# Kernel tuning notes

Measured on AMD Instinct MI355X. Metric: run time of the kernel, lower is better.

The kernel has to match this reference:

```python
import jax, jax.numpy as jnp
import numpy as np

D_MODEL = 1024
N_HEADS = 16
D_HEAD = D_MODEL // N_HEADS
D_FF = 2048
B, S = 4, 1024
EPS = 1e-6


def layernorm(x, gamma, beta):
    mu = jnp.mean(x, axis=-1, keepdims=True)
    var = jnp.mean(jnp.square(x - mu), axis=-1, keepdims=True)
    return (x - mu) * jax.lax.rsqrt(var + EPS) * gamma + beta


def setup_inputs() -> dict:
    key = jax.random.key(0)
    ks = jax.random.split(key, 12)
    s = 0.02
    return {
        "x": jax.random.normal(ks[0], (B, S, D_MODEL), jnp.float32),
        "mask": jnp.ones((B, 1, 1, S), jnp.int32),
        "Wq": jax.random.normal(ks[1], (D_MODEL, D_MODEL), jnp.float32) * s,
        "Wk": jax.random.normal(ks[2], (D_MODEL, D_MODEL), jnp.float32) * s,
        "Wv": jax.random.normal(ks[3], (D_MODEL, D_MODEL), jnp.float32) * s,
        "Wo": jax.random.normal(ks[4], (D_MODEL, D_MODEL), jnp.float32) * s,
        "bo": jnp.zeros((D_MODEL,), jnp.float32),
        "ln1_g": jnp.ones((D_MODEL,), jnp.float32),
        "ln1_b": jnp.zeros((D_MODEL,), jnp.float32),
        "W1": jax.random.normal(ks[5], (D_MODEL, D_FF), jnp.float32) * s,
        "b1": jnp.zeros((D_FF,), jnp.float32),
        "W2": jax.random.normal(ks[6], (D_FF, D_MODEL), jnp.float32) * s,
        "b2": jnp.zeros((D_MODEL,), jnp.float32),
        "ln2_g": jnp.ones((D_MODEL,), jnp.float32),
        "ln2_b": jnp.zeros((D_MODEL,), jnp.float32),
    }


def reference(x, mask, Wq, Wk, Wv, Wo, bo, ln1_g, ln1_b, W1, b1, W2, b2, ln2_g, ln2_b):
    b, s, _ = x.shape
    # --- multi-head attention ---
    q_proj = x @ Wq                      # [B,S,D]
    k_proj = x @ Wk
    v_proj = x @ Wv
    q = q_proj.reshape(b, s, N_HEADS, D_HEAD)
    k = k_proj.reshape(b, s, N_HEADS, D_HEAD)
    v = v_proj.reshape(b, s, N_HEADS, D_HEAD)
    attn = jnp.einsum('bqhd,bkhd->bhqk', q, k)           # [B,H,S,S]
    attn = jnp.where(mask == 0, -jnp.inf, attn)
    attn = jax.nn.softmax(attn / jnp.sqrt(jnp.float32(D_MODEL)), axis=-1)
    out = jnp.einsum('bhqk,bkhd->bqhd', attn, v).reshape(b, s, D_MODEL)
    # source applies ReLU after the output projection, dropout=eval identity
    out = jax.nn.relu(out @ Wo + bo) + q_proj            # residual = projected queries
    out = layernorm(out, ln1_g, ln1_b)
    # --- FFN (source applies activation AFTER linear2) ---
    ff = jax.nn.relu((out @ W1 + b1) @ W2 + b2) + out
    return layernorm(ff, ln2_g, ln2_b)
```

## Files before the change

kernel.cpp:

```cpp
#include <hip/hip_runtime.h>
#include <hip/hip_bf16.h>

#define D_MODEL 1024
#define N_HEADS 16
#define D_HEAD  64
#define D_FF    2048
#define BATCH   4
#define SEQ     1024
#define ROWS    (BATCH*SEQ)

typedef __bf16  bf16x8 __attribute__((ext_vector_type(8)));
typedef float   f32x4  __attribute__((ext_vector_type(4)));
typedef unsigned int u32x4 __attribute__((ext_vector_type(4)));
typedef unsigned int u32x2 __attribute__((ext_vector_type(2)));
typedef unsigned short u16;
typedef unsigned int u32;

__device__ inline u16 f2bf(float x){ __hip_bfloat16 b = __float2bfloat16(x); return *(u16*)&b; }

__device__ inline void load_lds16(const u16* gsrc, u16* ldst){
  __builtin_amdgcn_global_load_lds((const __attribute__((address_space(1))) void*)gsrc,
                                   (__attribute__((address_space(3))) void*)ldst, 16, 0, 0);
}

__global__ __launch_bounds__(256)
void cast_bf16_kernel(const float* __restrict__ src, __hip_bfloat16* __restrict__ dst, int n){
  int i = (blockIdx.x*blockDim.x + threadIdx.x)*4;
  if (i + 3 < n){
    float4 v = *(const float4*)(src + i);
    dst[i+0] = __float2bfloat16(v.x);
    dst[i+1] = __float2bfloat16(v.y);
    dst[i+2] = __float2bfloat16(v.z);
    dst[i+3] = __float2bfloat16(v.w);
  }
}

__global__ __launch_bounds__(256)
void transpose_cast_kernel(const float* __restrict__ src, __hip_bfloat16* __restrict__ dst,
                           int R, int C){
  __shared__ float tile[32][33];
  int c0 = blockIdx.x*32, r0 = blockIdx.y*32;
  int tx = threadIdx.x & 31, ty = threadIdx.x >> 5;
  #pragma unroll
  for (int i=0;i<32;i+=8)
    tile[ty+i][tx] = src[(size_t)(r0+ty+i)*C + (c0+tx)];
  __syncthreads();
  #pragma unroll
  for (int i=0;i<32;i+=8)
    dst[(size_t)(c0+ty+i)*R + (r0+tx)] = __float2bfloat16(tile[tx][ty+i]);
}

__global__ __launch_bounds__(256)
void transpose4_kernel(const float* __restrict__ s0, const float* __restrict__ s1,
                       const float* __restrict__ s2, const float* __restrict__ s3,
                       __hip_bfloat16* __restrict__ dst){
  __shared__ float tile[32][33];
  const float* src = (blockIdx.z==0)?s0:(blockIdx.z==1)?s1:(blockIdx.z==2)?s2:s3;
  __hip_bfloat16* d = dst + (size_t)blockIdx.z*1024*1024;
  int c0 = blockIdx.x*32, r0 = blockIdx.y*32;
  int tx = threadIdx.x & 31, ty = threadIdx.x >> 5;
  #pragma unroll
  for (int i=0;i<32;i+=8)
    tile[ty+i][tx] = src[(size_t)(r0+ty+i)*1024 + (c0+tx)];
  __syncthreads();
  #pragma unroll
  for (int i=0;i<32;i+=8)
    d[(size_t)(c0+ty+i)*1024 + (r0+tx)] = __float2bfloat16(tile[tx][ty+i]);
}

template<int MODE>
__global__ __launch_bounds__(256, 2)
void gemm_bt_kernel(const u16* __restrict__ A, const u16* __restrict__ BT,
                    const float* __restrict__ bias, float* __restrict__ Cf,
                    __hip_bfloat16* __restrict__ Cb, int M, int N, int K, float cscale){
  __shared__ u16 As[2][128*32];
  __shared__ u16 Bs[2][128*32];
  const int m0 = blockIdx.y*128, n0 = blockIdx.x*128;
  const int t = threadIdx.x;
  const int wid = t>>6, lane = t&63;
  const int wm = wid>>1, wn = wid&1;
  const int lr = lane&15, lk = (lane>>4)*8;
  const int srow = t>>2, sseg = (t&3)*8;
  const int wbase = wid*512;

  f32x4 acc[4][4] = {};

  for (int kt=0; kt<K; kt+=64){
    __syncthreads();
    #pragma unroll
    for (int half=0; half<2; ++half){
      #pragma unroll
      for (int c=0;c<2;++c){
        load_lds16(A  + (size_t)(m0 + c*64 + srow)*K + kt + half*32 + sseg, &As[half][c*2048 + wbase]);
        load_lds16(BT + (size_t)(n0 + c*64 + srow)*K + kt + half*32 + sseg, &Bs[half][c*2048 + wbase]);
      }
    }
    __syncthreads();
    #pragma unroll
    for (int half=0; half<2; ++half){
      bf16x8 af[4], bfr[4];
      #pragma unroll
      for (int f=0; f<4; ++f){
        af[f]  = *(const bf16x8*)&As[half][(wm*64 + f*16 + lr)*32 + lk];
        bfr[f] = *(const bf16x8*)&Bs[half][(wn*64 + f*16 + lr)*32 + lk];
      }
      #pragma unroll
      for (int i=0;i<4;++i)
        #pragma unroll
        for (int j=0;j<4;++j)
          acc[i][j] = __builtin_amdgcn_mfma_f32_16x16x32_bf16(af[i], bfr[j], acc[i][j], 0,0,0);
    }
  }

  const int r_in = (lane>>4)*4;
  #pragma unroll
  for (int i=0;i<4;++i){
    #pragma unroll
    for (int j=0;j<4;++j){
      int col = n0 + wn*64 + j*16 + lr;
      float bv = bias ? bias[col] : 0.f;
      #pragma unroll
      for (int e=0;e<4;++e){
        int row = m0 + wm*64 + i*16 + r_in + e;
        float v = acc[i][j][e] + bv;
        if (MODE == 0){
          Cf[(size_t)row*N + col] = v;
        } else if (MODE == 1){
          Cb[(size_t)row*N + col] = __float2bfloat16(v);
        } else {
          int b = row>>10, s = row&1023;
          int which = col>>10, c = col&1023, h = c>>6, d = c&63;
          size_t hm = (((size_t)b*16 + h)*1024 + s)*64 + d;
          if (which == 0){
            Cf[(size_t)row*1024 + c] = v;
            Cb[hm] = __float2bfloat16(v * cscale);
          } else if (which == 1){
            Cb[4194304u + hm] = __float2bfloat16(v);
          } else {
            Cb[8388608u + (((size_t)b*16 + h)*64 + d)*1024 + s] = __float2bfloat16(v);
          }
        }
      }
    }
  }
}

__global__ __launch_bounds__(512)
void attn_mfma_kernel(const u16* __restrict__ qb, const u16* __restrict__ kb,
                      const u16* __restrict__ vt, const int* __restrict__ mask,
                      __hip_bfloat16* __restrict__ out){
  __shared__ u16 Ks[64*72];
  __shared__ u16 Vs[64*72];
  __shared__ u16 Pl[8][16*72];
  const int t = threadIdx.x;
  const int wid = t>>6, lane = t&63;
  const int lr = lane&15, lg = lane>>4, lk = lg*8;
  const int bh = blockIdx.y;
  const int b = bh>>4, h = bh&15;
  const int q0 = blockIdx.x*128 + wid*16;
  const u16* qbase = qb + (size_t)bh*1024*64;
  const u16* kbase = kb + (size_t)bh*1024*64;
  const u16* vbase = vt + (size_t)bh*64*1024;
  const int* mrow = mask + b*SEQ;

  bf16x8 aq[2];
  aq[0] = *(const bf16x8*)(qbase + (size_t)(q0+lr)*64 + lk);
  aq[1] = *(const bf16x8*)(qbase + (size_t)(q0+lr)*64 + 32 + lk);

  f32x4 osum[4] = {};
  float m1 = -1e30f, l1 = 0.f;

  for (int kt=0; kt<SEQ/64; ++kt){
    const int k0 = kt*64;
    __syncthreads();
    {
      int r = t>>3, sg = (t&7)*8;
      *(u32x4*)&Ks[r*72+sg] = *(const u32x4*)(kbase + (size_t)(k0+r)*64 + sg);
      *(u32x4*)&Vs[r*72+sg] = *(const u32x4*)(vbase + (size_t)r*1024 + k0 + sg);
    }
    __syncthreads();

    unsigned long long bm = __ballot(mrow[k0 + lane] != 0);

    f32x4 sacc[4] = {};
    __builtin_amdgcn_s_setprio(1);
    #pragma unroll
    for (int k4=0;k4<4;++k4){
      #pragma unroll
      for (int dg=0;dg<2;++dg){
        bf16x8 kf = *(const bf16x8*)&Ks[(k4*16+lr)*72 + dg*32 + lk];
        sacc[k4] = __builtin_amdgcn_mfma_f32_16x16x32_bf16(kf, aq[dg], sacc[k4],0,0,0);
      }
    }
    __builtin_amdgcn_s_setprio(0);
    if (bm != ~0ull){
      #pragma unroll
      for (int k4=0;k4<4;++k4)
        #pragma unroll
        for (int e=0;e<4;++e)
          if (!((bm >> (k4*16 + lg*4 + e)) & 1)) sacc[k4][e] = -1e30f;
    }

    float tm = -1e30f;
    #pragma unroll
    for (int k4=0;k4<4;++k4)
      #pragma unroll
      for (int e=0;e<4;++e) tm = fmaxf(tm, sacc[k4][e]);
    tm = fmaxf(tm, __shfl_xor(tm,16));
    tm = fmaxf(tm, __shfl_xor(tm,32));

    float mn = m1, c = 1.f;
    bool need = !__all(tm <= m1 + 8.f);
    if (need){
      mn = fmaxf(m1, tm);
      c  = exp2f(m1 - mn);
      m1 = mn;
    }
    float ps = 0.f;
    #pragma unroll
    for (int k4=0;k4<4;++k4)
      #pragma unroll
      for (int e=0;e<4;++e){ float p = exp2f(sacc[k4][e]-mn); sacc[k4][e]=p; ps+=p; }
    ps += __shfl_xor(ps,16);
    ps += __shfl_xor(ps,32);
    l1 = l1*c + ps;

    if (need){
      float ce[4];
      #pragma unroll
      for (int e=0;e<4;++e) ce[e] = __shfl(c, lg*4+e);
      #pragma unroll
      for (int dt=0;dt<4;++dt)
        #pragma unroll
        for (int e=0;e<4;++e) osum[dt][e] *= ce[e];
    }

    #pragma unroll
    for (int k4=0;k4<4;++k4){
      u32 lo = (u32)f2bf(sacc[k4][0]) | ((u32)f2bf(sacc[k4][1])<<16);
      u32 hi = (u32)f2bf(sacc[k4][2]) | ((u32)f2bf(sacc[k4][3])<<16);
      u32x2 pk; pk[0]=lo; pk[1]=hi;
      *(u32x2*)&Pl[wid][lr*72 + k4*16 + lg*4] = pk;
    }
    __builtin_amdgcn_s_setprio(1);
    #pragma unroll
    for (int dt=0;dt<4;++dt){
      #pragma unroll
      for (int kg=0;kg<2;++kg){
        bf16x8 pa = *(const bf16x8*)&Pl[wid][lr*72 + kg*32 + lk];
        bf16x8 vf = *(const bf16x8*)&Vs[(dt*16+lr)*72 + kg*32 + lk];
        osum[dt] = __builtin_amdgcn_mfma_f32_16x16x32_bf16(pa, vf, osum[dt],0,0,0);
      }
    }
    __builtin_amdgcn_s_setprio(0);
  }
  float li[4];
  #pragma unroll
  for (int e=0;e<4;++e) li[e] = 1.f / __shfl(l1, lg*4+e);
  #pragma unroll
  for (int dt=0;dt<4;++dt){
    int d = dt*16 + lr;
    #pragma unroll
    for (int e=0;e<4;++e){
      int q = q0 + lg*4 + e;
      out[((size_t)b*1024 + q)*1024 + h*64 + d] = __float2bfloat16(osum[dt][e] * li[e]);
    }
  }
}

__global__ __launch_bounds__(256)
void ln_fused_kernel(const float* __restrict__ a, const float* __restrict__ res,
                     const float* __restrict__ g, const float* __restrict__ be,
                     float* __restrict__ outf, __hip_bfloat16* __restrict__ outb){
  int row = blockIdx.x, t = threadIdx.x;
  size_t rb = (size_t)row*D_MODEL;
  float4 av = *(const float4*)(a  + rb + t*4);
  float4 rv = *(const float4*)(res+ rb + t*4);
  float v0 = fmaxf(av.x,0.f)+rv.x;
  float v1 = fmaxf(av.y,0.f)+rv.y;
  float v2 = fmaxf(av.z,0.f)+rv.z;
  float v3 = fmaxf(av.w,0.f)+rv.w;
  float sum = v0+v1+v2+v3;
  float ss  = v0*v0+v1*v1+v2*v2+v3*v3;
  #pragma unroll
  for (int off=32; off; off>>=1){ sum += __shfl_xor(sum,off); ss += __shfl_xor(ss,off); }
  __shared__ float red[8];
  int wid = t>>6, lane = t&63;
  if (lane==0){ red[wid]=sum; red[4+wid]=ss; }
  __syncthreads();
  sum = red[0]+red[1]+red[2]+red[3];
  ss  = red[4]+red[5]+red[6]+red[7];
  float mu  = sum*(1.f/1024.f);
  float var = ss*(1.f/1024.f) - mu*mu;
  float rstd = rsqrtf(var + 1e-6f);
  float4 gv = *(const float4*)(g  + t*4);
  float4 bv = *(const float4*)(be + t*4);
  float y0=(v0-mu)*rstd*gv.x+bv.x;
  float y1=(v1-mu)*rstd*gv.y+bv.y;
  float y2=(v2-mu)*rstd*gv.z+bv.z;
  float y3=(v3-mu)*rstd*gv.w+bv.w;
  *(float4*)(outf+rb+t*4) = make_float4(y0,y1,y2,y3);
  if (outb){
    outb[rb+t*4+0]=__float2bfloat16(y0);
    outb[rb+t*4+1]=__float2bfloat16(y1);
    outb[rb+t*4+2]=__float2bfloat16(y2);
    outb[rb+t*4+3]=__float2bfloat16(y3);
  }
}

extern "C" void kernel_launch(void* const* d_in, const int* in_sizes, int n_in,
                              void* d_out, int out_size, void* d_ws, size_t ws_size,
                              hipStream_t stream){
  const float* x    = (const float*)d_in[0];
  const int*   mask = (const int*)  d_in[1];
  const float* Wq   = (const float*)d_in[2];
  const float* Wk   = (const float*)d_in[3];
  const float* Wv   = (const float*)d_in[4];
  const float* Wo   = (const float*)d_in[5];
  const float* bo   = (const float*)d_in[6];
  const float* ln1g = (const float*)d_in[7];
  const float* ln1b = (const float*)d_in[8];
  const float* W1   = (const float*)d_in[9];
  const float* b1   = (const float*)d_in[10];
  const float* W2   = (const float*)d_in[11];
  const float* b2   = (const float*)d_in[12];
  const float* ln2g = (const float*)d_in[13];
  const float* ln2b = (const float*)d_in[14];

  char* ws = (char*)d_ws;
  const size_t MB = 1024*1024;
  __hip_bfloat16* WqT  = (__hip_bfloat16*)(ws + 0);
  __hip_bfloat16* WoT  = (__hip_bfloat16*)(ws + 6*MB);
  __hip_bfloat16* W1T  = (__hip_bfloat16*)(ws + 8*MB);
  __hip_bfloat16* W2T  = (__hip_bfloat16*)(ws + 12*MB);
  __hip_bfloat16* xb   = (__hip_bfloat16*)(ws + 16*MB);
  float* q_proj        = (float*)(ws + 24*MB);
  __hip_bfloat16* qb   = (__hip_bfloat16*)(ws + 40*MB);
  __hip_bfloat16* attn_o = (__hip_bfloat16*)(ws + 64*MB);
  float* proj_o        = (float*)(ws + 40*MB);
  float* h1f           = (float*)(ws + 56*MB);
  __hip_bfloat16* h1b  = (__hip_bfloat16*)(ws + 16*MB);
  __hip_bfloat16* ff1b = (__hip_bfloat16*)(ws + 24*MB);
  float* ff2           = (float*)(ws + 40*MB);

  const float qscale = 0.03125f * 1.44269504f;

  cast_bf16_kernel<<<ROWS*D_MODEL/4/256, 256, 0, stream>>>(x, xb, ROWS*D_MODEL);
  transpose4_kernel<<<dim3(32,32,4), 256, 0, stream>>>(Wq, Wk, Wv, Wo, WqT);
  transpose_cast_kernel<<<dim3(64,32), 256, 0, stream>>>(W1, W1T, 1024, 2048);
  transpose_cast_kernel<<<dim3(32,64), 256, 0, stream>>>(W2, W2T, 2048, 1024);

  gemm_bt_kernel<5><<<dim3(24,32), 256, 0, stream>>>((const u16*)xb, (const u16*)WqT, nullptr,
                                                     q_proj, qb, ROWS, 3072, 1024, qscale);

  attn_mfma_kernel<<<dim3(SEQ/128, BATCH*N_HEADS), 512, 0, stream>>>(
      (const u16*)qb, (const u16*)(qb + 4194304u), (const u16*)(qb + 8388608u), mask, attn_o);

  gemm_bt_kernel<0><<<dim3(8,32), 256, 0, stream>>>((const u16*)attn_o, (const u16*)WoT, bo,
                                                    proj_o, nullptr, ROWS, 1024, 1024, 1.f);

  ln_fused_kernel<<<ROWS, 256, 0, stream>>>(proj_o, q_proj, ln1g, ln1b, h1f, h1b);

  gemm_bt_kernel<1><<<dim3(16,32), 256, 0, stream>>>((const u16*)h1b, (const u16*)W1T, b1,
                                                     nullptr, ff1b, ROWS, 2048, 1024, 1.f);

  gemm_bt_kernel<0><<<dim3(8,32), 256, 0, stream>>>((const u16*)ff1b, (const u16*)W2T, b2,
                                                    ff2, nullptr, ROWS, 1024, 2048, 1.f);

  ln_fused_kernel<<<ROWS, 256, 0, stream>>>(ff2, h1f, ln2g, ln2b, (float*)d_out, nullptr);
}
```

Baseline: 215.7 us.

## Double-buffer attention K/V tiles, remap blocks per XCD, fuse ReLU+residual into GEMM

The attention kernel now double-buffers its K/V tiles in LDS. Each iteration prefetches the next tile into registers and writes it to the alternate buffer after the MFMA work, so only one barrier is needed per iteration. The attention grid is flattened and remapped so that the blocks of one (batch, head) land on the same XCD, which is meant to improve L2 reuse of K/V. The ReLU-plus-residual step moves from the layernorm kernel into a new GEMM epilogue mode, so layernorm no longer reads the residual tensor. In exchange, the attention kernel uses more LDS and registers, and the GEMM epilogue does an extra residual load.

```diff
diff --git a/kernel.cpp b/kernel.cpp
--- a/kernel.cpp
+++ b/kernel.cpp
@@ -71,8 +71,9 @@
 template<int MODE>
 __global__ __launch_bounds__(256, 2)
 void gemm_bt_kernel(const u16* __restrict__ A, const u16* __restrict__ BT,
-                    const float* __restrict__ bias, float* __restrict__ Cf,
-                    __hip_bfloat16* __restrict__ Cb, int M, int N, int K, float cscale){
+                    const float* __restrict__ bias, const float* __restrict__ res,
+                    float* __restrict__ Cf, __hip_bfloat16* __restrict__ Cb,
+                    int M, int N, int K, float cscale){
   __shared__ u16 As[2][128*32];
   __shared__ u16 Bs[2][128*32];
   const int m0 = blockIdx.y*128, n0 = blockIdx.x*128;
@@ -127,6 +128,8 @@
           Cf[(size_t)row*N + col] = v;
         } else if (MODE == 1){
           Cb[(size_t)row*N + col] = __float2bfloat16(v);
+        } else if (MODE == 6){
+          Cf[(size_t)row*N + col] = fmaxf(v,0.f) + res[(size_t)row*N + col];
         } else {
           int b = row>>10, s = row&1023;
           int which = col>>10, c = col&1023, h = c>>6, d = c&63;
@@ -149,15 +152,18 @@
 void attn_mfma_kernel(const u16* __restrict__ qb, const u16* __restrict__ kb,
                       const u16* __restrict__ vt, const int* __restrict__ mask,
                       __hip_bfloat16* __restrict__ out){
-  __shared__ u16 Ks[64*72];
-  __shared__ u16 Vs[64*72];
+  __shared__ u16 Ks[2][64*72];
+  __shared__ u16 Vs[2][64*72];
   __shared__ u16 Pl[8][16*72];
   const int t = threadIdx.x;
   const int wid = t>>6, lane = t&63;
   const int lr = lane&15, lg = lane>>4, lk = lg*8;
-  const int bh = blockIdx.y;
+  const int bid = blockIdx.x;
+  const int xcd = bid & 7, slot = bid >> 3;
+  const int bh = xcd*8 + (slot>>3);
+  const int qx = slot & 7;
   const int b = bh>>4, h = bh&15;
-  const int q0 = blockIdx.x*128 + wid*16;
+  const int q0 = qx*128 + wid*16;
   const u16* qbase = qb + (size_t)bh*1024*64;
   const u16* kbase = kb + (size_t)bh*1024*64;
   const u16* vbase = vt + (size_t)bh*64*1024;
@@ -170,15 +176,24 @@
   f32x4 osum[4] = {};
   float m1 = -1e30f, l1 = 0.f;
 
+  const int sr = t>>3, sg = (t&7)*8;
+  {
+    u32x4 kr = *(const u32x4*)(kbase + (size_t)sr*64 + sg);
+    u32x4 vr = *(const u32x4*)(vbase + (size_t)sr*1024 + sg);
+    *(u32x4*)&Ks[0][sr*72+sg] = kr;
+    *(u32x4*)&Vs[0][sr*72+sg] = vr;
+  }
+  __syncthreads();
+
   for (int kt=0; kt<SEQ/64; ++kt){
     const int k0 = kt*64;
-    __syncthreads();
-    {
-      int r = t>>3, sg = (t&7)*8;
-      *(u32x4*)&Ks[r*72+sg] = *(const u32x4*)(kbase + (size_t)(k0+r)*64 + sg);
-      *(u32x4*)&Vs[r*72+sg] = *(const u32x4*)(vbase + (size_t)r*1024 + k0 + sg);
-    }
-    __syncthreads();
+    const int cur = kt&1;
+    u32x4 kr, vr;
+    const bool more = (kt+1 < SEQ/64);
+    if (more){
+      kr = *(const u32x4*)(kbase + (size_t)(k0+64+sr)*64 + sg);
+      vr = *(const u32x4*)(vbase + (size_t)sr*1024 + (k0+64) + sg);
+    }
 
     unsigned long long bm = __ballot(mrow[k0 + lane] != 0);
 
@@ -188,7 +203,7 @@
     for (int k4=0;k4<4;++k4){
       #pragma unroll
       for (int dg=0;dg<2;++dg){
-        bf16x8 kf = *(const bf16x8*)&Ks[(k4*16+lr)*72 + dg*32 + lk];
+        bf16x8 kf = *(const bf16x8*)&Ks[cur][(k4*16+lr)*72 + dg*32 + lk];
         sacc[k4] = __builtin_amdgcn_mfma_f32_16x16x32_bf16(kf, aq[dg], sacc[k4],0,0,0);
       }
     }
@@ -248,11 +263,17 @@
       #pragma unroll
       for (int kg=0;kg<2;++kg){
         bf16x8 pa = *(const bf16x8*)&Pl[wid][lr*72 + kg*32 + lk];
-        bf16x8 vf = *(const bf16x8*)&Vs[(dt*16+lr)*72 + kg*32 + lk];
+        bf16x8 vf = *(const bf16x8*)&Vs[cur][(dt*16+lr)*72 + kg*32 + lk];
         osum[dt] = __builtin_amdgcn_mfma_f32_16x16x32_bf16(pa, vf, osum[dt],0,0,0);
       }
     }
     __builtin_amdgcn_s_setprio(0);
+
+    if (more){
+      *(u32x4*)&Ks[cur^1][sr*72+sg] = kr;
+      *(u32x4*)&Vs[cur^1][sr*72+sg] = vr;
+    }
+    __syncthreads();
   }
   float li[4];
   #pragma unroll
@@ -269,17 +290,13 @@
 }
 
 __global__ __launch_bounds__(256)
-void ln_fused_kernel(const float* __restrict__ a, const float* __restrict__ res,
-                     const float* __restrict__ g, const float* __restrict__ be,
-                     float* __restrict__ outf, __hip_bfloat16* __restrict__ outb){
+void ln_kernel(const float* __restrict__ a, const float* __restrict__ g,
+               const float* __restrict__ be, float* __restrict__ outf,
+               __hip_bfloat16* __restrict__ outb){
   int row = blockIdx.x, t = threadIdx.x;
   size_t rb = (size_t)row*D_MODEL;
-  float4 av = *(const float4*)(a  + rb + t*4);
-  float4 rv = *(const float4*)(res+ rb + t*4);
-  float v0 = fmaxf(av.x,0.f)+rv.x;
-  float v1 = fmaxf(av.y,0.f)+rv.y;
-  float v2 = fmaxf(av.z,0.f)+rv.z;
-  float v3 = fmaxf(av.w,0.f)+rv.w;
+  float4 av = *(const float4*)(a + rb + t*4);
+  float v0 = av.x, v1 = av.y, v2 = av.z, v3 = av.w;
   float sum = v0+v1+v2+v3;
   float ss  = v0*v0+v1*v1+v2*v2+v3*v3;
   #pragma unroll
@@ -337,11 +354,11 @@
   float* q_proj        = (float*)(ws + 24*MB);
   __hip_bfloat16* qb   = (__hip_bfloat16*)(ws + 40*MB);
   __hip_bfloat16* attn_o = (__hip_bfloat16*)(ws + 64*MB);
-  float* proj_o        = (float*)(ws + 40*MB);
+  float* t1f           = (float*)(ws + 40*MB);
   float* h1f           = (float*)(ws + 56*MB);
   __hip_bfloat16* h1b  = (__hip_bfloat16*)(ws + 16*MB);
   __hip_bfloat16* ff1b = (__hip_bfloat16*)(ws + 24*MB);
-  float* ff2           = (float*)(ws + 40*MB);
+  float* t2f           = (float*)(ws + 40*MB);
 
   const float qscale = 0.03125f * 1.44269504f;
 
@@ -351,21 +368,21 @@
   transpose_cast_kernel<<<dim3(32,64), 256, 0, stream>>>(W2, W2T, 2048, 1024);
 
   gemm_bt_kernel<5><<<dim3(24,32), 256, 0, stream>>>((const u16*)xb, (const u16*)WqT, nullptr,
-                                                     q_proj, qb, ROWS, 3072, 1024, qscale);
-
-  attn_mfma_kernel<<<dim3(SEQ/128, BATCH*N_HEADS), 512, 0, stream>>>(
+                                                     nullptr, q_proj, qb, ROWS, 3072, 1024, qscale);
+
+  attn_mfma_kernel<<<512, 512, 0, stream>>>(
       (const u16*)qb, (const u16*)(qb + 4194304u), (const u16*)(qb + 8388608u), mask, attn_o);
 
-  gemm_bt_kernel<0><<<dim3(8,32), 256, 0, stream>>>((const u16*)attn_o, (const u16*)WoT, bo,
-                                                    proj_o, nullptr, ROWS, 1024, 1024, 1.f);
-
-  ln_fused_kernel<<<ROWS, 256, 0, stream>>>(proj_o, q_proj, ln1g, ln1b, h1f, h1b);
+  gemm_bt_kernel<6><<<dim3(8,32), 256, 0, stream>>>((const u16*)attn_o, (const u16*)WoT, bo,
+                                                    q_proj, t1f, nullptr, ROWS, 1024, 1024, 1.f);
+
+  ln_kernel<<<ROWS, 256, 0, stream>>>(t1f, ln1g, ln1b, h1f, h1b);
 
   gemm_bt_kernel<1><<<dim3(16,32), 256, 0, stream>>>((const u16*)h1b, (const u16*)W1T, b1,
-                                                     nullptr, ff1b, ROWS, 2048, 1024, 1.f);
-
-  gemm_bt_kernel<0><<<dim3(8,32), 256, 0, stream>>>((const u16*)ff1b, (const u16*)W2T, b2,
-                                                    ff2, nullptr, ROWS, 1024, 2048, 1.f);
-
-  ln_fused_kernel<<<ROWS, 256, 0, stream>>>(ff2, h1f, ln2g, ln2b, (float*)d_out, nullptr);
-}
+                                                     nullptr, nullptr, ff1b, ROWS, 2048, 1024, 1.f);
+
+  gemm_bt_kernel<6><<<dim3(8,32), 256, 0, stream>>>((const u16*)ff1b, (const u16*)W2T, b2,
+                                                    h1f, t2f, nullptr, ROWS, 1024, 2048, 1.f);
+
+  ln_kernel<<<ROWS, 256, 0, stream>>>(t2f, ln2g, ln2b, (float*)d_out, nullptr);
+}
```

Result: faster. 209.1 us (-3.0%).
